# Kernel optimization log

Measured on AMD Instinct MI355X. Metric: run time of the kernel, lower is better.

Reference implementation:

```python
import jax, jax.numpy as jnp
import numpy as np

N_NODES = 100000
N_EDGES = 3200000
IN_DIM = 512
OUT_DIM = 3


def _sage_conv(x, src, dst, ll_w, ll_b, lr_w):
    # PyG SAGEConv (mean aggr): out = lin_l(mean_{j in N(i)} x_j) + lin_r(x_i)
    n = x.shape[0]
    msgs = x[src]                                            # [E, d_in]
    agg = jax.ops.segment_sum(msgs, dst, num_segments=n)      # [N, d_in]
    cnt = jax.ops.segment_sum(jnp.ones((src.shape[0],), x.dtype), dst, num_segments=n)
    mean = agg / jnp.maximum(cnt, 1.0)[:, None]
    return mean @ ll_w + ll_b + x @ lr_w


def setup_inputs() -> dict:
    key = jax.random.key(0)
    ks = jax.random.split(key, 16)
    d = {}
    d["x"] = jax.random.normal(ks[0], (N_NODES, IN_DIM), dtype=jnp.float32)
    d["edge_index"] = jax.random.randint(ks[1], (2, N_EDGES), 0, N_NODES, dtype=jnp.int64)
    s = lambda fan_in: 1.0 / np.sqrt(fan_in)
    d["fc1_w"] = jax.random.uniform(ks[2], (IN_DIM, 16), jnp.float32, -s(IN_DIM), s(IN_DIM))
    d["fc1_b"] = jax.random.uniform(ks[3], (16,), jnp.float32, -s(IN_DIM), s(IN_DIM))
    d["conv1_ll_w"] = jax.random.uniform(ks[4], (16, 32), jnp.float32, -s(16), s(16))
    d["conv1_ll_b"] = jnp.zeros((32,), jnp.float32)
    d["conv1_lr_w"] = jax.random.uniform(ks[5], (16, 32), jnp.float32, -s(16), s(16))
    d["conv2_ll_w"] = jax.random.uniform(ks[6], (32, 16), jnp.float32, -s(32), s(32))
    d["conv2_ll_b"] = jnp.zeros((16,), jnp.float32)
    d["conv2_lr_w"] = jax.random.uniform(ks[7], (32, 16), jnp.float32, -s(32), s(32))
    d["fc2_w"] = jax.random.uniform(ks[8], (16, OUT_DIM), jnp.float32, -s(16), s(16))
    d["fc2_b"] = jax.random.uniform(ks[9], (OUT_DIM,), jnp.float32, -s(16), s(16))
    return d


def reference(x, edge_index, fc1_w, fc1_b, conv1_ll_w, conv1_ll_b, conv1_lr_w,
              conv2_ll_w, conv2_ll_b, conv2_lr_w, fc2_w, fc2_b):
    src, dst = edge_index[0], edge_index[1]
    h = jax.nn.relu(x @ fc1_w + fc1_b)                              # [N, 16]
    h = jax.nn.relu(_sage_conv(h, src, dst, conv1_ll_w, conv1_ll_b, conv1_lr_w))  # [N, 32]
    h = jax.nn.relu(_sage_conv(h, src, dst, conv2_ll_w, conv2_ll_b, conv2_lr_w))  # [N, 16]
    h = h @ fc2_w + fc2_b                                           # [N, 3]
    gsi = jax.nn.sigmoid(h[:, 1])
    mxi = jax.nn.sigmoid(h[:, 2])
    fsi = jax.nn.relu(h[:, 0]) + gsi
    return jnp.stack([fsi, gsi, mxi], axis=1)
```

## Files before the change

### kernel.cpp

```cpp
#include <hip/hip_runtime.h>
#include <math.h>

#define N_NODES 100000
#define N_EDGES 3200000
#define BSHIFT 8
#define NPB 256
#define BMASK (NPB - 1)
#define NB 391
#define CAP 10240
#define FC1_BLOCKS 1536
#define STG_BLOCKS 512

typedef __attribute__((ext_vector_type(8))) short short8v;
typedef __attribute__((ext_vector_type(4))) float f32x4;

__device__ inline unsigned cvt_pk_bf16(float a, float b) {
  unsigned r;
  asm("v_cvt_pk_bf16_f32 %0, %1, %2" : "=v"(r) : "v"(a), "v"(b));
  return r;
}
__device__ inline unsigned short f32_to_bf16(float f) {
  union { float f; unsigned u; } v; v.f = f;
  unsigned r = v.u + 0x7fff + ((v.u >> 16) & 1);
  return (unsigned short)(r >> 16);
}
__device__ inline float bf16_to_f32(unsigned short h) {
  union { unsigned u; float f; } v; v.u = ((unsigned)h) << 16;
  return v.f;
}

__global__ __launch_bounds__(256) void fc1_stage_kernel(
    const float* __restrict__ x, const float* __restrict__ w,
    const float* __restrict__ b, unsigned short* __restrict__ h1,
    const int* __restrict__ src, const int* __restrict__ dst,
    int* __restrict__ gcur, int* __restrict__ staged) {
  __shared__ int hist[NB], base[NB];
  __shared__ short8v wlds[16][64];

  if (blockIdx.x < FC1_BLOCKS) {
    const int lane = threadIdx.x & 63;
    const int o = lane & 15;
    const int kb = lane >> 4;
    const int wid = (blockIdx.x * 256 + threadIdx.x) >> 6;
    const int nwaves = FC1_BLOCKS * 4;

    for (int idx = threadIdx.x; idx < 4096; idx += 256) {
      const int s = idx >> 8, ln = (idx >> 2) & 63, j = idx & 3;
      const int lkb = ln >> 4, lo = ln & 15;
      const int k = s * 32 + lkb * 8 + 2 * j;
      ((unsigned*)&wlds[s][ln])[j] =
          cvt_pk_bf16(w[(size_t)k * 16 + lo], w[(size_t)(k + 1) * 16 + lo]);
    }
    __syncthreads();

    const float bias = b[o];
    const int ntiles = N_NODES / 16;

    for (int tile = wid; tile < ntiles; tile += nwaves) {
      const float* xrow = x + (size_t)(tile * 16 + o) * 512 + kb * 8;
      f32x4 c = {0.f, 0.f, 0.f, 0.f};
#pragma unroll
      for (int s = 0; s < 16; ++s) {
        const float4* xp = (const float4*)(xrow + s * 32);
        float4 a0 = xp[0];
        float4 a1 = xp[1];
        union { unsigned u[4]; short8v v; } fa;
        fa.u[0] = cvt_pk_bf16(a0.x, a0.y);
        fa.u[1] = cvt_pk_bf16(a0.z, a0.w);
        fa.u[2] = cvt_pk_bf16(a1.x, a1.y);
        fa.u[3] = cvt_pk_bf16(a1.z, a1.w);
        c = __builtin_amdgcn_mfma_f32_16x16x32_bf16(fa.v, wlds[s][lane], c,
                                                    0, 0, 0);
      }
      const int rbase = tile * 16 + (lane >> 4) * 4;
#pragma unroll
      for (int j = 0; j < 4; ++j) {
        h1[(size_t)(rbase + j) * 16 + o] = f32_to_bf16(fmaxf(c[j] + bias, 0.f));
      }
    }
  } else {
    const int tid = threadIdx.x;
    for (int i = tid; i < NB; i += 256) hist[i] = 0;
    __syncthreads();

    const int sb = blockIdx.x - FC1_BLOCKS;
    const int per = (N_EDGES + STG_BLOCKS - 1) / STG_BLOCKS;
    const int e0 = sb * per;
    const int e1 = min(e0 + per, N_EDGES);

    for (int e = e0 + tid; e < e1; e += 256) {
      atomicAdd(&hist[dst[e] >> BSHIFT], 1);
    }
    __syncthreads();
    for (int bkt = tid; bkt < NB; bkt += 256) {
      int h = hist[bkt];
      base[bkt] = (h > 0) ? atomicAdd(&gcur[bkt], h) : 0;
      hist[bkt] = 0;
    }
    __syncthreads();
    for (int e = e0 + tid; e < e1; e += 256) {
      int d = dst[e];
      int s = src[e];
      int bkt = d >> BSHIFT;
      int pos = base[bkt] + atomicAdd(&hist[bkt], 1);
      if (pos < CAP) staged[bkt * CAP + pos] = (s << 8) | (d & BMASK);
    }
  }
}

__global__ __launch_bounds__(256) void finalize_kernel(
    int* __restrict__ staged, const int* __restrict__ gcur,
    int* __restrict__ offs, int* __restrict__ cnt) {
  __shared__ int ed[CAP];
  __shared__ int lcnt[NPB];
  __shared__ int lofs[NPB];
  __shared__ int sc[256];
  const int bkt = blockIdx.x, tid = threadIdx.x;
  const int nE = min(gcur[bkt], CAP);
  const int base = bkt * CAP;
  for (int e = tid; e < nE; e += 256) ed[e] = staged[base + e];
  lcnt[tid] = 0;
  __syncthreads();
  for (int e = tid; e < nE; e += 256) atomicAdd(&lcnt[ed[e] & BMASK], 1);
  __syncthreads();
  const int v = lcnt[tid];
  sc[tid] = v;
  __syncthreads();
  for (int d = 1; d < 256; d <<= 1) {
    int add = (tid >= d) ? sc[tid - d] : 0;
    __syncthreads();
    sc[tid] += add;
    __syncthreads();
  }
  const int excl = sc[tid] - v;
  lofs[tid] = excl;
  const int g = bkt * NPB + tid;
  if (g < N_NODES) {
    offs[g] = base + excl;
    cnt[g] = v;
  }
  lcnt[tid] = 0;
  __syncthreads();
  for (int e = tid; e < nE; e += 256) {
    int u = ed[e];
    int dl = u & BMASK;
    int pos = lofs[dl] + atomicAdd(&lcnt[dl], 1);
    staged[base + pos] = u >> 8;
  }
}

__global__ __launch_bounds__(256) void conv1_kernel(
    const unsigned short* __restrict__ h1, const int* __restrict__ csr,
    const int* __restrict__ offs, const int* __restrict__ cnt,
    const float* __restrict__ llw, const float* __restrict__ llb,
    const float* __restrict__ lrw, const float* __restrict__ c2llw,
    float* __restrict__ h2, unsigned short* __restrict__ t2) {
  __shared__ float wl[512], wr[512], w2c[512];
  __shared__ float bb[32];
  for (int idx = threadIdx.x; idx < 512; idx += 256) {
    const int k = idx >> 5, jj = idx & 31;
    const int sj = 4 * ((jj >> 2) ^ (k >> 2)) + (jj & 3);
    wl[k * 32 + sj] = llw[idx];
    wr[k * 32 + sj] = lrw[idx];
    w2c[idx] = c2llw[idx];
  }
  if (threadIdx.x < 32) bb[threadIdx.x] = llb[threadIdx.x];
  __syncthreads();

  const int tid = blockIdx.x * 256 + threadIdx.x;
  const int i = tid >> 3;
  if (i >= N_NODES) return;
  const int t8 = threadIdx.x & 7;
  const int gg = t8 >> 2;
  const int t = t8 & 3;
  const int start = offs[i], deg = cnt[i];

  float4 acc = make_float4(0.f, 0.f, 0.f, 0.f);
  int e = gg;
  for (; e + 6 < deg; e += 8) {
    const int s0 = csr[start + e];
    const int s1 = csr[start + e + 2];
    const int s2 = csr[start + e + 4];
    const int s3 = csr[start + e + 6];
    ushort4 a0 = *(const ushort4*)(h1 + (size_t)s0 * 16 + t * 4);
    ushort4 a1 = *(const ushort4*)(h1 + (size_t)s1 * 16 + t * 4);
    ushort4 a2 = *(const ushort4*)(h1 + (size_t)s2 * 16 + t * 4);
    ushort4 a3 = *(const ushort4*)(h1 + (size_t)s3 * 16 + t * 4);
    acc.x += (bf16_to_f32(a0.x) + bf16_to_f32(a1.x)) +
             (bf16_to_f32(a2.x) + bf16_to_f32(a3.x));
    acc.y += (bf16_to_f32(a0.y) + bf16_to_f32(a1.y)) +
             (bf16_to_f32(a2.y) + bf16_to_f32(a3.y));
    acc.z += (bf16_to_f32(a0.z) + bf16_to_f32(a1.z)) +
             (bf16_to_f32(a2.z) + bf16_to_f32(a3.z));
    acc.w += (bf16_to_f32(a0.w) + bf16_to_f32(a1.w)) +
             (bf16_to_f32(a2.w) + bf16_to_f32(a3.w));
  }
  for (; e < deg; e += 2) {
    const int s = csr[start + e];
    ushort4 a = *(const ushort4*)(h1 + (size_t)s * 16 + t * 4);
    acc.x += bf16_to_f32(a.x); acc.y += bf16_to_f32(a.y);
    acc.z += bf16_to_f32(a.z); acc.w += bf16_to_f32(a.w);
  }
  acc.x += __shfl_xor(acc.x, 4, 64);
  acc.y += __shfl_xor(acc.y, 4, 64);
  acc.z += __shfl_xor(acc.z, 4, 64);
  acc.w += __shfl_xor(acc.w, 4, 64);

  const float inv = 1.f / (float)(deg > 0 ? deg : 1);
  const ushort4 selfu = *(const ushort4*)(h1 + (size_t)i * 16 + t * 4);
  const float mk[4] = {acc.x * inv, acc.y * inv, acc.z * inv, acc.w * inv};
  const float sk[4] = {bf16_to_f32(selfu.x), bf16_to_f32(selfu.y),
                       bf16_to_f32(selfu.z), bf16_to_f32(selfu.w)};

  float4 p[8];
#pragma unroll
  for (int q = 0; q < 8; ++q) p[q] = make_float4(0.f, 0.f, 0.f, 0.f);
#pragma unroll
  for (int j = 0; j < 4; ++j) {
    const int k = 4 * t + j;
#pragma unroll
    for (int q = 0; q < 8; ++q) {
      const int qs = 4 * (q ^ t);
      float4 w4l = *(const float4*)&wl[k * 32 + qs];
      float4 w4r = *(const float4*)&wr[k * 32 + qs];
      p[q].x += mk[j] * w4l.x + sk[j] * w4r.x;
      p[q].y += mk[j] * w4l.y + sk[j] * w4r.y;
      p[q].z += mk[j] * w4l.z + sk[j] * w4r.z;
      p[q].w += mk[j] * w4l.w + sk[j] * w4r.w;
    }
  }
#pragma unroll
  for (int mask = 1; mask <= 2; mask <<= 1) {
#pragma unroll
    for (int q = 0; q < 8; ++q) {
      p[q].x += __shfl_xor(p[q].x, mask, 64);
      p[q].y += __shfl_xor(p[q].y, mask, 64);
      p[q].z += __shfl_xor(p[q].z, mask, 64);
      p[q].w += __shfl_xor(p[q].w, mask, 64);
    }
  }
  float o[32];
#pragma unroll
  for (int q = 0; q < 8; ++q) {
    o[4 * q + 0] = fmaxf(p[q].x + bb[4 * q + 0], 0.f);
    o[4 * q + 1] = fmaxf(p[q].y + bb[4 * q + 1], 0.f);
    o[4 * q + 2] = fmaxf(p[q].z + bb[4 * q + 2], 0.f);
    o[4 * q + 3] = fmaxf(p[q].w + bb[4 * q + 3], 0.f);
  }
  *(float4*)(h2 + (size_t)i * 32 + 4 * t8) =
      make_float4(o[4 * t8], o[4 * t8 + 1], o[4 * t8 + 2], o[4 * t8 + 3]);
  float t0 = 0.f, t1 = 0.f;
#pragma unroll
  for (int k = 0; k < 32; ++k) {
    const float ok = o[k];
    t0 += ok * w2c[k * 16 + 2 * t8];
    t1 += ok * w2c[k * 16 + 2 * t8 + 1];
  }
  *(unsigned*)(t2 + (size_t)i * 16 + 2 * t8) = cvt_pk_bf16(t0, t1);
}

__global__ __launch_bounds__(256) void conv2_kernel(
    const unsigned short* __restrict__ t2, const float* __restrict__ h2,
    const int* __restrict__ csr, const int* __restrict__ offs,
    const int* __restrict__ cnt, const float* __restrict__ llb,
    const float* __restrict__ lrw, const float* __restrict__ fc2w,
    const float* __restrict__ fc2b, float* __restrict__ out) {
  __shared__ float wr[512];
  __shared__ float bb[16];
  __shared__ float w2[48];
  __shared__ float b2[3];
  for (int idx = threadIdx.x; idx < 512; idx += 256) {
    const int k = idx >> 4, jj = idx & 15;
    const int sj = 4 * ((jj >> 2) ^ ((k >> 2) & 3)) + (jj & 3);
    wr[k * 16 + sj] = lrw[idx];
  }
  if (threadIdx.x < 16) bb[threadIdx.x] = llb[threadIdx.x];
  else if (threadIdx.x >= 64 && threadIdx.x < 112) w2[threadIdx.x - 64] = fc2w[threadIdx.x - 64];
  else if (threadIdx.x >= 128 && threadIdx.x < 131) b2[threadIdx.x - 128] = fc2b[threadIdx.x - 128];
  __syncthreads();

  const int tid = blockIdx.x * 256 + threadIdx.x;
  const int i = tid >> 3;
  if (i >= N_NODES) return;
  const int t8 = threadIdx.x & 7;
  const int gg = t8 >> 2;
  const int t = t8 & 3;
  const int start = offs[i], deg = cnt[i];

  float4 acc = make_float4(0.f, 0.f, 0.f, 0.f);
  int e = gg;
  for (; e + 6 < deg; e += 8) {
    const int s0 = csr[start + e];
    const int s1 = csr[start + e + 2];
    const int s2 = csr[start + e + 4];
    const int s3 = csr[start + e + 6];
    ushort4 a0 = *(const ushort4*)(t2 + (size_t)s0 * 16 + t * 4);
    ushort4 a1 = *(const ushort4*)(t2 + (size_t)s1 * 16 + t * 4);
    ushort4 a2 = *(const ushort4*)(t2 + (size_t)s2 * 16 + t * 4);
    ushort4 a3 = *(const ushort4*)(t2 + (size_t)s3 * 16 + t * 4);
    acc.x += (bf16_to_f32(a0.x) + bf16_to_f32(a1.x)) +
             (bf16_to_f32(a2.x) + bf16_to_f32(a3.x));
    acc.y += (bf16_to_f32(a0.y) + bf16_to_f32(a1.y)) +
             (bf16_to_f32(a2.y) + bf16_to_f32(a3.y));
    acc.z += (bf16_to_f32(a0.z) + bf16_to_f32(a1.z)) +
             (bf16_to_f32(a2.z) + bf16_to_f32(a3.z));
    acc.w += (bf16_to_f32(a0.w) + bf16_to_f32(a1.w)) +
             (bf16_to_f32(a2.w) + bf16_to_f32(a3.w));
  }
  for (; e < deg; e += 2) {
    const int s = csr[start + e];
    ushort4 a = *(const ushort4*)(t2 + (size_t)s * 16 + t * 4);
    acc.x += bf16_to_f32(a.x); acc.y += bf16_to_f32(a.y);
    acc.z += bf16_to_f32(a.z); acc.w += bf16_to_f32(a.w);
  }
  acc.x += __shfl_xor(acc.x, 4, 64);
  acc.y += __shfl_xor(acc.y, 4, 64);
  acc.z += __shfl_xor(acc.z, 4, 64);
  acc.w += __shfl_xor(acc.w, 4, 64);

  const float inv = 1.f / (float)(deg > 0 ? deg : 1);
  const float4 s0v = *(const float4*)(h2 + (size_t)i * 32 + 4 * t8);
  const float sk[4] = {s0v.x, s0v.y, s0v.z, s0v.w};
  float4 p[4];
#pragma unroll
  for (int q = 0; q < 4; ++q) p[q] = make_float4(0.f, 0.f, 0.f, 0.f);
#pragma unroll
  for (int kk = 0; kk < 4; ++kk) {
    const int k = 4 * t8 + kk;
    const float s = sk[kk];
#pragma unroll
    for (int q = 0; q < 4; ++q) {
      const int qs = 4 * (q ^ (t8 & 3));
      const float4 wv = *(const float4*)&wr[k * 16 + qs];
      p[q].x += s * wv.x; p[q].y += s * wv.y;
      p[q].z += s * wv.z; p[q].w += s * wv.w;
    }
  }
  if (gg == 0) {
    p[t].x += acc.x * inv; p[t].y += acc.y * inv;
    p[t].z += acc.z * inv; p[t].w += acc.w * inv;
  }
#pragma unroll
  for (int mask = 1; mask <= 4; mask <<= 1) {
#pragma unroll
    for (int q = 0; q < 4; ++q) {
      p[q].x += __shfl_xor(p[q].x, mask, 64);
      p[q].y += __shfl_xor(p[q].y, mask, 64);
      p[q].z += __shfl_xor(p[q].z, mask, 64);
      p[q].w += __shfl_xor(p[q].w, mask, 64);
    }
  }
  if (t8 < 3) {
    float f[16];
#pragma unroll
    for (int q = 0; q < 4; ++q) {
      f[4 * q + 0] = fmaxf(p[q].x + bb[4 * q + 0], 0.f);
      f[4 * q + 1] = fmaxf(p[q].y + bb[4 * q + 1], 0.f);
      f[4 * q + 2] = fmaxf(p[q].z + bb[4 * q + 2], 0.f);
      f[4 * q + 3] = fmaxf(p[q].w + bb[4 * q + 3], 0.f);
    }
    float v0 = b2[0], v1 = b2[1], v2 = b2[2];
#pragma unroll
    for (int k = 0; k < 16; ++k) {
      v0 += f[k] * w2[k * 3 + 0];
      v1 += f[k] * w2[k * 3 + 1];
      v2 += f[k] * w2[k * 3 + 2];
    }
    float gsi = 1.f / (1.f + expf(-v1));
    float mxi = 1.f / (1.f + expf(-v2));
    float fsi = fmaxf(v0, 0.f) + gsi;
    float rv = (t8 == 0) ? fsi : ((t8 == 1) ? gsi : mxi);
    out[(size_t)i * 3 + t8] = rv;
  }
}

extern "C" void kernel_launch(void* const* d_in, const int* in_sizes, int n_in,
                              void* d_out, int out_size, void* d_ws, size_t ws_size,
                              hipStream_t stream) {
  const float* x = (const float*)d_in[0];
  const int* ei = (const int*)d_in[1];
  const float* fc1w = (const float*)d_in[2];
  const float* fc1b = (const float*)d_in[3];
  const float* c1llw = (const float*)d_in[4];
  const float* c1llb = (const float*)d_in[5];
  const float* c1lrw = (const float*)d_in[6];
  const float* c2llw = (const float*)d_in[7];
  const float* c2llb = (const float*)d_in[8];
  const float* c2lrw = (const float*)d_in[9];
  const float* fc2w = (const float*)d_in[10];
  const float* fc2b = (const float*)d_in[11];
  float* outp = (float*)d_out;
  const int* src = ei;
  const int* dst = ei + N_EDGES;

  char* ws = (char*)d_ws;
  unsigned short* h1 = (unsigned short*)ws;  ws += (size_t)N_NODES * 16 * 2;
  float* h2 = (float*)ws;                    ws += (size_t)N_NODES * 32 * 4;
  unsigned short* t2 = (unsigned short*)ws;  ws += (size_t)N_NODES * 16 * 2;
  int* staged = (int*)ws;                    ws += (size_t)NB * CAP * 4;
  int* gcur = (int*)ws;                      ws += (size_t)NB * 4;
  int* offs = (int*)ws;                      ws += (size_t)N_NODES * 4;
  int* cnt = (int*)ws;                       ws += (size_t)N_NODES * 4;
  (void)ws_size; (void)n_in; (void)in_sizes; (void)out_size;

  hipMemsetAsync(gcur, 0, (size_t)NB * 4, stream);
  fc1_stage_kernel<<<FC1_BLOCKS + STG_BLOCKS, 256, 0, stream>>>(
      x, fc1w, fc1b, h1, src, dst, gcur, staged);
  finalize_kernel<<<NB, 256, 0, stream>>>(staged, gcur, offs, cnt);
  conv1_kernel<<<(N_NODES * 8 + 255) / 256, 256, 0, stream>>>(
      h1, staged, offs, cnt, c1llw, c1llb, c1lrw, c2llw, h2, t2);
  conv2_kernel<<<(N_NODES * 8 + 255) / 256, 256, 0, stream>>>(
      t2, h2, staged, offs, cnt, c2llb, c2lrw, fc2w, fc2b, outp);
}
```

Measured before the change: 220.8 us.

## Split fused fc1/edge-staging kernel into two sequential kernels

```diff
diff --git a/kernel.cpp b/kernel.cpp
--- a/kernel.cpp
+++ b/kernel.cpp
@@ -8,8 +8,8 @@
 #define BMASK (NPB - 1)
 #define NB 391
 #define CAP 10240
-#define FC1_BLOCKS 1536
-#define STG_BLOCKS 512
+#define FC1_GRID 768
+#define STG_GRID 512
 
 typedef __attribute__((ext_vector_type(8))) short short8v;
 typedef __attribute__((ext_vector_type(4))) float f32x4;
@@ -29,82 +29,86 @@
   return v.f;
 }
 
-__global__ __launch_bounds__(256) void fc1_stage_kernel(
+__global__ __launch_bounds__(256) void fc1_kernel(
     const float* __restrict__ x, const float* __restrict__ w,
-    const float* __restrict__ b, unsigned short* __restrict__ h1,
+    const float* __restrict__ b, unsigned short* __restrict__ h1) {
+  __shared__ float wraw[512 * 16];
+  __shared__ short8v wlds[16][64];
+
+  for (int idx = threadIdx.x; idx < 2048; idx += 256) {
+    ((float4*)wraw)[idx] = ((const float4*)w)[idx];
+  }
+  __syncthreads();
+  for (int idx = threadIdx.x; idx < 4096; idx += 256) {
+    const int s = idx >> 8, ln = (idx >> 2) & 63, j = idx & 3;
+    const int lkb = ln >> 4, lo = ln & 15;
+    const int k = s * 32 + lkb * 8 + 2 * j;
+    ((unsigned*)&wlds[s][ln])[j] =
+        cvt_pk_bf16(wraw[k * 16 + lo], wraw[(k + 1) * 16 + lo]);
+  }
+  __syncthreads();
+
+  const int lane = threadIdx.x & 63;
+  const int o = lane & 15;
+  const int kb = lane >> 4;
+  const int wid = (blockIdx.x * 256 + threadIdx.x) >> 6;
+  const int nwaves = FC1_GRID * 4;
+  const float bias = b[o];
+  const int ntiles = N_NODES / 16;
+
+  for (int tile = wid; tile < ntiles; tile += nwaves) {
+    const float* xrow = x + (size_t)(tile * 16 + o) * 512 + kb * 8;
+    f32x4 c = {0.f, 0.f, 0.f, 0.f};
+#pragma unroll
+    for (int s = 0; s < 16; ++s) {
+      const float4* xp = (const float4*)(xrow + s * 32);
+      float4 a0 = xp[0];
+      float4 a1 = xp[1];
+      union { unsigned u[4]; short8v v; } fa;
+      fa.u[0] = cvt_pk_bf16(a0.x, a0.y);
+      fa.u[1] = cvt_pk_bf16(a0.z, a0.w);
+      fa.u[2] = cvt_pk_bf16(a1.x, a1.y);
+      fa.u[3] = cvt_pk_bf16(a1.z, a1.w);
+      c = __builtin_amdgcn_mfma_f32_16x16x32_bf16(fa.v, wlds[s][lane], c,
+                                                  0, 0, 0);
+    }
+    const int rbase = tile * 16 + (lane >> 4) * 4;
+#pragma unroll
+    for (int j = 0; j < 4; ++j) {
+      h1[(size_t)(rbase + j) * 16 + o] = f32_to_bf16(fmaxf(c[j] + bias, 0.f));
+    }
+  }
+}
+
+__global__ __launch_bounds__(256) void stage_kernel(
     const int* __restrict__ src, const int* __restrict__ dst,
     int* __restrict__ gcur, int* __restrict__ staged) {
-  __shared__ int hist[NB], base[NB];
-  __shared__ short8v wlds[16][64];
-
-  if (blockIdx.x < FC1_BLOCKS) {
-    const int lane = threadIdx.x & 63;
-    const int o = lane & 15;
-    const int kb = lane >> 4;
-    const int wid = (blockIdx.x * 256 + threadIdx.x) >> 6;
-    const int nwaves = FC1_BLOCKS * 4;
-
-    for (int idx = threadIdx.x; idx < 4096; idx += 256) {
-      const int s = idx >> 8, ln = (idx >> 2) & 63, j = idx & 3;
-      const int lkb = ln >> 4, lo = ln & 15;
-      const int k = s * 32 + lkb * 8 + 2 * j;
-      ((unsigned*)&wlds[s][ln])[j] =
-          cvt_pk_bf16(w[(size_t)k * 16 + lo], w[(size_t)(k + 1) * 16 + lo]);
-    }
-    __syncthreads();
-
-    const float bias = b[o];
-    const int ntiles = N_NODES / 16;
-
-    for (int tile = wid; tile < ntiles; tile += nwaves) {
-      const float* xrow = x + (size_t)(tile * 16 + o) * 512 + kb * 8;
-      f32x4 c = {0.f, 0.f, 0.f, 0.f};
-#pragma unroll
-      for (int s = 0; s < 16; ++s) {
-        const float4* xp = (const float4*)(xrow + s * 32);
-        float4 a0 = xp[0];
-        float4 a1 = xp[1];
-        union { unsigned u[4]; short8v v; } fa;
-        fa.u[0] = cvt_pk_bf16(a0.x, a0.y);
-        fa.u[1] = cvt_pk_bf16(a0.z, a0.w);
-        fa.u[2] = cvt_pk_bf16(a1.x, a1.y);
-        fa.u[3] = cvt_pk_bf16(a1.z, a1.w);
-        c = __builtin_amdgcn_mfma_f32_16x16x32_bf16(fa.v, wlds[s][lane], c,
-                                                    0, 0, 0);
-      }
-      const int rbase = tile * 16 + (lane >> 4) * 4;
-#pragma unroll
-      for (int j = 0; j < 4; ++j) {
-        h1[(size_t)(rbase + j) * 16 + o] = f32_to_bf16(fmaxf(c[j] + bias, 0.f));
-      }
-    }
-  } else {
-    const int tid = threadIdx.x;
-    for (int i = tid; i < NB; i += 256) hist[i] = 0;
-    __syncthreads();
-
-    const int sb = blockIdx.x - FC1_BLOCKS;
-    const int per = (N_EDGES + STG_BLOCKS - 1) / STG_BLOCKS;
-    const int e0 = sb * per;
-    const int e1 = min(e0 + per, N_EDGES);
-
-    for (int e = e0 + tid; e < e1; e += 256) {
-      atomicAdd(&hist[dst[e] >> BSHIFT], 1);
-    }
-    __syncthreads();
-    for (int bkt = tid; bkt < NB; bkt += 256) {
-      int h = hist[bkt];
-      base[bkt] = (h > 0) ? atomicAdd(&gcur[bkt], h) : 0;
-      hist[bkt] = 0;
-    }
-    __syncthreads();
-    for (int e = e0 + tid; e < e1; e += 256) {
-      int d = dst[e];
-      int s = src[e];
-      int bkt = d >> BSHIFT;
-      int pos = base[bkt] + atomicAdd(&hist[bkt], 1);
-      if (pos < CAP) staged[bkt * CAP + pos] = (s << 8) | (d & BMASK);
-    }
+  __shared__ int hist[NB];
+  __shared__ int base[NB];
+  const int tid = threadIdx.x;
+  for (int i = tid; i < NB; i += 256) hist[i] = 0;
+  __syncthreads();
+
+  const int per = (N_EDGES + STG_GRID - 1) / STG_GRID;
+  const int e0 = blockIdx.x * per;
+  const int e1 = min(e0 + per, N_EDGES);
+
+  for (int e = e0 + tid; e < e1; e += 256) {
+    atomicAdd(&hist[dst[e] >> BSHIFT], 1);
+  }
+  __syncthreads();
+  for (int bkt = tid; bkt < NB; bkt += 256) {
+    int h = hist[bkt];
+    base[bkt] = (h > 0) ? atomicAdd(&gcur[bkt], h) : 0;
+    hist[bkt] = 0;
+  }
+  __syncthreads();
+  for (int e = e0 + tid; e < e1; e += 256) {
+    int d = dst[e];
+    int s = src[e];
+    int bkt = d >> BSHIFT;
+    int pos = base[bkt] + atomicAdd(&hist[bkt], 1);
+    if (pos < CAP) staged[bkt * CAP + pos] = (s << 8) | (d & BMASK);
   }
 }
 
@@ -404,8 +408,8 @@
   (void)ws_size; (void)n_in; (void)in_sizes; (void)out_size;
 
   hipMemsetAsync(gcur, 0, (size_t)NB * 4, stream);
-  fc1_stage_kernel<<<FC1_BLOCKS + STG_BLOCKS, 256, 0, stream>>>(
-      x, fc1w, fc1b, h1, src, dst, gcur, staged);
+  stage_kernel<<<STG_GRID, 256, 0, stream>>>(src, dst, gcur, staged);
+  fc1_kernel<<<FC1_GRID, 256, 0, stream>>>(x, fc1w, fc1b, h1);
   finalize_kernel<<<NB, 256, 0, stream>>>(staged, gcur, offs, cnt);
   conv1_kernel<<<(N_NODES * 8 + 255) / 256, 256, 0, stream>>>(
       h1, staged, offs, cnt, c1llw, c1llb, c1lrw, c2llw, h2, t2);
```

Result: slower. 237.2 us (+7.4%).

## Stage fc1 input tiles through swizzled LDS with coalesced loads

Applied to the files above, without the earlier changes.

```diff
diff --git a/kernel.cpp b/kernel.cpp
--- a/kernel.cpp
+++ b/kernel.cpp
@@ -8,7 +8,7 @@
 #define BMASK (NPB - 1)
 #define NB 391
 #define CAP 10240
-#define FC1_BLOCKS 1536
+#define FC1_BLOCKS 512
 #define STG_BLOCKS 512
 
 typedef __attribute__((ext_vector_type(8))) short short8v;
@@ -34,15 +34,16 @@
     const float* __restrict__ b, unsigned short* __restrict__ h1,
     const int* __restrict__ src, const int* __restrict__ dst,
     int* __restrict__ gcur, int* __restrict__ staged) {
-  __shared__ int hist[NB], base[NB];
-  __shared__ short8v wlds[16][64];
+  __shared__ __align__(16) char smem[81920];
 
   if (blockIdx.x < FC1_BLOCKS) {
+    short8v (*wlds)[64] = (short8v(*)[64])smem;
     const int lane = threadIdx.x & 63;
+    const int wib = threadIdx.x >> 6;
+    char* mybuf = smem + 16384 + wib * 16384;
     const int o = lane & 15;
     const int kb = lane >> 4;
-    const int wid = (blockIdx.x * 256 + threadIdx.x) >> 6;
-    const int nwaves = FC1_BLOCKS * 4;
+    const int xorv = (o & 7) << 4;
 
     for (int idx = threadIdx.x; idx < 4096; idx += 256) {
       const int s = idx >> 8, ln = (idx >> 2) & 63, j = idx & 3;
@@ -55,30 +56,55 @@
 
     const float bias = b[o];
     const int ntiles = N_NODES / 16;
-
-    for (int tile = wid; tile < ntiles; tile += nwaves) {
-      const float* xrow = x + (size_t)(tile * 16 + o) * 512 + kb * 8;
-      f32x4 c = {0.f, 0.f, 0.f, 0.f};
-#pragma unroll
-      for (int s = 0; s < 16; ++s) {
-        const float4* xp = (const float4*)(xrow + s * 32);
-        float4 a0 = xp[0];
-        float4 a1 = xp[1];
-        union { unsigned u[4]; short8v v; } fa;
-        fa.u[0] = cvt_pk_bf16(a0.x, a0.y);
-        fa.u[1] = cvt_pk_bf16(a0.z, a0.w);
-        fa.u[2] = cvt_pk_bf16(a1.x, a1.y);
-        fa.u[3] = cvt_pk_bf16(a1.z, a1.w);
-        c = __builtin_amdgcn_mfma_f32_16x16x32_bf16(fa.v, wlds[s][lane], c,
-                                                    0, 0, 0);
+    const int nwaves = FC1_BLOCKS * 4;
+
+    for (int t0 = blockIdx.x * 4; t0 < ntiles; t0 += nwaves) {
+      const int tile = t0 + wib;
+      const bool active = tile < ntiles;
+
+      if (active) {
+        const float4* xt = (const float4*)x + (size_t)tile * 2048;
+#pragma unroll
+        for (int cch = 0; cch < 4; ++cch) {
+          float4 v[8];
+#pragma unroll
+          for (int j = 0; j < 8; ++j) {
+            v[j] = xt[(cch * 8 + j) * 64 + lane];
+          }
+#pragma unroll
+          for (int j = 0; j < 8; ++j) {
+            const int f = (cch * 8 + j) * 64 + lane;
+            const int row = f >> 7, col8 = f & 127;
+            uint2 pk;
+            pk.x = cvt_pk_bf16(v[j].x, v[j].y);
+            pk.y = cvt_pk_bf16(v[j].z, v[j].w);
+            *(uint2*)(mybuf + row * 1024 + ((col8 * 8) ^ ((row & 7) << 4))) = pk;
+          }
+        }
       }
-      const int rbase = tile * 16 + (lane >> 4) * 4;
-#pragma unroll
-      for (int j = 0; j < 4; ++j) {
-        h1[(size_t)(rbase + j) * 16 + o] = f32_to_bf16(fmaxf(c[j] + bias, 0.f));
+      __syncthreads();
+
+      if (active) {
+        f32x4 c = {0.f, 0.f, 0.f, 0.f};
+#pragma unroll
+        for (int s = 0; s < 16; ++s) {
+          const short8v a =
+              *(const short8v*)(mybuf + o * 1024 + ((kb * 16 + s * 64) ^ xorv));
+          c = __builtin_amdgcn_mfma_f32_16x16x32_bf16(a, wlds[s][lane], c,
+                                                      0, 0, 0);
+        }
+        const int rbase = tile * 16 + (lane >> 4) * 4;
+#pragma unroll
+        for (int j = 0; j < 4; ++j) {
+          h1[(size_t)(rbase + j) * 16 + o] =
+              f32_to_bf16(fmaxf(c[j] + bias, 0.f));
+        }
       }
+      __syncthreads();
     }
   } else {
+    int* hist = (int*)smem;
+    int* base = (int*)(smem + 2048);
     const int tid = threadIdx.x;
     for (int i = tid; i < NB; i += 256) hist[i] = 0;
     __syncthreads();
```

New measurement: 224.9 us. No clear change (+1.8%).

## Stage fc1 input tiles into LDS via direct global-to-LDS loads with split-K waves

Applied to the files above, without the earlier changes.

```diff
diff --git a/kernel.cpp b/kernel.cpp
--- a/kernel.cpp
+++ b/kernel.cpp
@@ -8,11 +8,14 @@
 #define BMASK (NPB - 1)
 #define NB 391
 #define CAP 10240
-#define FC1_BLOCKS 1536
 #define STG_BLOCKS 512
+#define FC1_BLOCKS 2048
+#define NTILES 6250
 
 typedef __attribute__((ext_vector_type(8))) short short8v;
 typedef __attribute__((ext_vector_type(4))) float f32x4;
+typedef __attribute__((address_space(3))) unsigned lds_u32;
+typedef const __attribute__((address_space(1))) unsigned glb_u32;
 
 __device__ inline unsigned cvt_pk_bf16(float a, float b) {
   unsigned r;
@@ -34,56 +37,89 @@
     const float* __restrict__ b, unsigned short* __restrict__ h1,
     const int* __restrict__ src, const int* __restrict__ dst,
     int* __restrict__ gcur, int* __restrict__ staged) {
-  __shared__ int hist[NB], base[NB];
-  __shared__ short8v wlds[16][64];
-
-  if (blockIdx.x < FC1_BLOCKS) {
-    const int lane = threadIdx.x & 63;
+  __shared__ __align__(16) char smem[53248];
+
+  if (blockIdx.x >= STG_BLOCKS) {
+    float* tile = (float*)smem;
+    short8v (*wlds)[64] = (short8v(*)[64])(smem + 32768);
+    f32x4* pbuf = (f32x4*)(smem + 49152);
+    const int tid = threadIdx.x;
+    const int lane = tid & 63;
+    const int wib = tid >> 6;
     const int o = lane & 15;
     const int kb = lane >> 4;
-    const int wid = (blockIdx.x * 256 + threadIdx.x) >> 6;
-    const int nwaves = FC1_BLOCKS * 4;
-
-    for (int idx = threadIdx.x; idx < 4096; idx += 256) {
+
+    for (int i = tid; i < 2048; i += 256)
+      ((float4*)tile)[i] = ((const float4*)w)[i];
+    __syncthreads();
+    for (int idx = tid; idx < 4096; idx += 256) {
       const int s = idx >> 8, ln = (idx >> 2) & 63, j = idx & 3;
       const int lkb = ln >> 4, lo = ln & 15;
       const int k = s * 32 + lkb * 8 + 2 * j;
       ((unsigned*)&wlds[s][ln])[j] =
-          cvt_pk_bf16(w[(size_t)k * 16 + lo], w[(size_t)(k + 1) * 16 + lo]);
+          cvt_pk_bf16(tile[k * 16 + lo], tile[(k + 1) * 16 + lo]);
     }
     __syncthreads();
 
     const float bias = b[o];
-    const int ntiles = N_NODES / 16;
-
-    for (int tile = wid; tile < ntiles; tile += nwaves) {
-      const float* xrow = x + (size_t)(tile * 16 + o) * 512 + kb * 8;
-      f32x4 c = {0.f, 0.f, 0.f, 0.f};
-#pragma unroll
-      for (int s = 0; s < 16; ++s) {
-        const float4* xp = (const float4*)(xrow + s * 32);
-        float4 a0 = xp[0];
-        float4 a1 = xp[1];
+    const int fcb = blockIdx.x - STG_BLOCKS;
+
+    for (int tileid = fcb; tileid < NTILES; tileid += FC1_BLOCKS) {
+      const float* xbase = x + (size_t)tileid * 8192;
+#pragma unroll
+      for (int i = 0; i < 8; ++i) {
+        const int c = wib * 8 + i;
+        const int r = c >> 1;
+        const int off = (c & 1) * 1024 + lane * 16;
+        const int goff = off ^ ((r & 7) << 5);
+        __builtin_amdgcn_global_load_lds(
+            (glb_u32*)(xbase + r * 512 + (goff >> 2)),
+            (lds_u32*)((char*)tile + (size_t)c * 1024 + lane * 16) - lane * 4,
+            16, 0, 0);
+      }
+      __syncthreads();
+
+      f32x4 c4 = {0.f, 0.f, 0.f, 0.f};
+#pragma unroll
+      for (int ss = 0; ss < 4; ++ss) {
+        const int s = wib * 4 + ss;
+        const int cb = (s * 128 + kb * 32) ^ ((o & 7) << 5);
+        const char* p = (const char*)tile + o * 2048 + cb;
+        const float4 a0 = *(const float4*)p;
+        const float4 a1 = *(const float4*)(p + 16);
         union { unsigned u[4]; short8v v; } fa;
         fa.u[0] = cvt_pk_bf16(a0.x, a0.y);
         fa.u[1] = cvt_pk_bf16(a0.z, a0.w);
         fa.u[2] = cvt_pk_bf16(a1.x, a1.y);
         fa.u[3] = cvt_pk_bf16(a1.z, a1.w);
-        c = __builtin_amdgcn_mfma_f32_16x16x32_bf16(fa.v, wlds[s][lane], c,
-                                                    0, 0, 0);
+        c4 = __builtin_amdgcn_mfma_f32_16x16x32_bf16(fa.v, wlds[s][lane], c4,
+                                                     0, 0, 0);
       }
-      const int rbase = tile * 16 + (lane >> 4) * 4;
-#pragma unroll
-      for (int j = 0; j < 4; ++j) {
-        h1[(size_t)(rbase + j) * 16 + o] = f32_to_bf16(fmaxf(c[j] + bias, 0.f));
+      pbuf[wib * 64 + lane] = c4;
+      __syncthreads();
+      if (wib == 0) {
+        const f32x4 p0 = pbuf[lane];
+        const f32x4 p1 = pbuf[64 + lane];
+        const f32x4 p2 = pbuf[128 + lane];
+        const f32x4 p3 = pbuf[192 + lane];
+        const int rbase = tileid * 16 + (lane >> 4) * 4;
+#pragma unroll
+        for (int j = 0; j < 4; ++j) {
+          const float vj = (p0[j] + p1[j]) + (p2[j] + p3[j]);
+          h1[(size_t)(rbase + j) * 16 + o] =
+              f32_to_bf16(fmaxf(vj + bias, 0.f));
+        }
       }
+      __syncthreads();
     }
   } else {
+    int* hist = (int*)smem;
+    int* base = (int*)(smem + 2048);
     const int tid = threadIdx.x;
     for (int i = tid; i < NB; i += 256) hist[i] = 0;
     __syncthreads();
 
-    const int sb = blockIdx.x - FC1_BLOCKS;
+    const int sb = blockIdx.x;
     const int per = (N_EDGES + STG_BLOCKS - 1) / STG_BLOCKS;
     const int e0 = sb * per;
     const int e1 = min(e0 + per, N_EDGES);
@@ -404,7 +440,7 @@
   (void)ws_size; (void)n_in; (void)in_sizes; (void)out_size;
 
   hipMemsetAsync(gcur, 0, (size_t)NB * 4, stream);
-  fc1_stage_kernel<<<FC1_BLOCKS + STG_BLOCKS, 256, 0, stream>>>(
+  fc1_stage_kernel<<<STG_BLOCKS + FC1_BLOCKS, 256, 0, stream>>>(
       x, fc1w, fc1b, h1, src, dst, gcur, staged);
   finalize_kernel<<<NB, 256, 0, stream>>>(staged, gcur, offs, cnt);
   conv1_kernel<<<(N_NODES * 8 + 255) / 256, 256, 0, stream>>>(
```

Result: faster. 215.4 us (-2.5%).
